# Performance work log

Measured on AMD Instinct MI355X. Metric: run time of the kernel, lower is better.

Reference implementation:

```python
import jax, jax.numpy as jnp
import numpy as np

N_NODES = 100000
N_EDGES = 1600000
DIM = 128
K_LAYERS = 3


def setup_inputs() -> dict:
    key = jax.random.key(0)
    ks = jax.random.split(key, 6)
    x = jax.random.normal(ks[0], (N_NODES, DIM), dtype=jnp.float32)
    edge_index = jax.random.randint(ks[1], (2, N_EDGES), 0, N_NODES, dtype=jnp.int64)
    scale = 1.0 / np.sqrt(DIM)
    W1 = jax.random.normal(ks[2], (K_LAYERS, DIM, DIM), dtype=jnp.float32) * scale
    b1 = jnp.zeros((K_LAYERS, DIM), dtype=jnp.float32)
    W2 = jax.random.normal(ks[3], (K_LAYERS, DIM, DIM), dtype=jnp.float32) * scale
    b2 = jnp.zeros((K_LAYERS, DIM), dtype=jnp.float32)
    return {"x": x, "edge_index": edge_index, "W1": W1, "b1": b1, "W2": W2, "b2": b2}


def reference(x, edge_index, W1, b1, W2, b2):
    # GINConv (PyG, eps=0): out = MLP(x + sum_{j -> i} x_j)
    src = edge_index[0]  # message source nodes (x_j)
    dst = edge_index[1]  # aggregation targets
    n = x.shape[0]
    for i in range(K_LAYERS):
        agg = jax.ops.segment_sum(x[src], dst, num_segments=n)  # [N, D]
        h = x + agg                                             # (1+eps)*x + agg, eps=0
        h = jax.nn.relu(h @ W1[i] + b1[i])
        x = h @ W2[i] + b2[i]
    return x
```

## Files before the change

kernel.cpp:

```cpp
#include <hip/hip_runtime.h>
#include <hip/hip_bf16.h>
#include <cstddef>

#define DIM_C 128
typedef unsigned short ushort_t;
typedef unsigned int uint_t;

constexpr int TILE_N = 64;
constexpr int BLOCK  = 256;
constexpr int HP2    = DIM_C + 8;
constexpr int CAP    = 64;

typedef __attribute__((ext_vector_type(8))) short bf16x8;
typedef __attribute__((ext_vector_type(4))) float f32x4;
typedef int intx4 __attribute__((ext_vector_type(4)));

__device__ inline ushort_t f2bf(float x) {
    __hip_bfloat16 h = __float2bfloat16(x);
    return *reinterpret_cast<ushort_t*>(&h);
}

constexpr int NGRP   = 8;
constexpr int NCHUNK = 256;
constexpr int NB_BKT = NGRP * NCHUNK;

__global__ __launch_bounds__(256)
void prep_all(const int* __restrict__ srcv, const int* __restrict__ dstv,
              int E, int N, int* __restrict__ cnt, int* __restrict__ col,
              const float* __restrict__ x, ushort_t* __restrict__ xb,
              const float* __restrict__ W1, const float* __restrict__ W2,
              ushort_t* __restrict__ Wt1, ushort_t* __restrict__ Wt2,
              int n8, int per)
{
    if (blockIdx.x < NB_BKT) {
        const int grp   = blockIdx.x & (NGRP - 1);
        const int chunk = blockIdx.x >> 3;
        const int RW = (N + NGRP - 1) / NGRP;
        const int lo = grp * RW;
        const int Q  = E >> 2;
        const int QP = (Q + NCHUNK - 1) / NCHUNK;
        const int q0 = chunk * QP;
        const int q1 = min(Q, q0 + QP);
        const intx4* d4p = (const intx4*)dstv;
        const intx4* s4p = (const intx4*)srcv;

        for (int q = q0 + threadIdx.x; q < q1; q += 256) {
            intx4 d = __builtin_nontemporal_load(&d4p[q]);
            const bool a0 = (unsigned)(d.x - lo) < (unsigned)RW;
            const bool a1 = (unsigned)(d.y - lo) < (unsigned)RW;
            const bool a2 = (unsigned)(d.z - lo) < (unsigned)RW;
            const bool a3 = (unsigned)(d.w - lo) < (unsigned)RW;
            if (a0 | a1 | a2 | a3) {
                intx4 s = __builtin_nontemporal_load(&s4p[q]);
                int p;
                if (a0) { p = atomicAdd(&cnt[d.x], 1); if (p < CAP) col[(size_t)d.x * CAP + p] = s.x; }
                if (a1) { p = atomicAdd(&cnt[d.y], 1); if (p < CAP) col[(size_t)d.y * CAP + p] = s.y; }
                if (a2) { p = atomicAdd(&cnt[d.z], 1); if (p < CAP) col[(size_t)d.z * CAP + p] = s.z; }
                if (a3) { p = atomicAdd(&cnt[d.w], 1); if (p < CAP) col[(size_t)d.w * CAP + p] = s.w; }
            }
        }
        if (chunk == 0) {
            for (int e = (Q << 2) + threadIdx.x; e < E; e += 256) {
                int dd = dstv[e];
                if ((unsigned)(dd - lo) < (unsigned)RW) {
                    int p = atomicAdd(&cnt[dd], 1);
                    if (p < CAP) col[(size_t)dd * CAP + p] = srcv[e];
                }
            }
        }
    } else {
        int i = (blockIdx.x - NB_BKT) * 256 + threadIdx.x;
        if (i < n8) {
            float4 a = ((const float4*)x)[2 * i];
            float4 b = ((const float4*)x)[2 * i + 1];
            union { ushort_t us[8]; uint4 u; } pk;
            pk.us[0] = f2bf(a.x); pk.us[1] = f2bf(a.y); pk.us[2] = f2bf(a.z); pk.us[3] = f2bf(a.w);
            pk.us[4] = f2bf(b.x); pk.us[5] = f2bf(b.y); pk.us[6] = f2bf(b.z); pk.us[7] = f2bf(b.w);
            ((uint4*)xb)[i] = pk.u;
        } else {
            int idx = i - n8;
            if (idx < 2 * per) {
                const float* src = (idx < per) ? W1 : W2;
                ushort_t* dst    = (idx < per) ? Wt1 : Wt2;
                int r = (idx < per) ? idx : idx - per;
                int l = r >> 14, rr = r & 16383, n = rr >> 7, k = rr & 127;
                dst[r] = f2bf(src[(l << 14) + (k << 7) + n]);
            }
        }
    }
}

__device__ inline void acc_bf8(float* acc, uint4 v) {
    uint_t w[4] = {v.x, v.y, v.z, v.w};
    #pragma unroll
    for (int k = 0; k < 4; ++k) {
        acc[2 * k]     += __uint_as_float(w[k] << 16);
        acc[2 * k + 1] += __uint_as_float(w[k] & 0xffff0000u);
    }
}

template <int U>
__device__ inline void gq(float* acc, const ushort_t* __restrict__ xb,
                          int cc, int qb, int j, int lq) {
    int cs[U];
    #pragma unroll
    for (int u = 0; u < U; ++u) cs[u] = __shfl(cc, qb + j + u);
    uint4 v[U];
    #pragma unroll
    for (int u = 0; u < U; ++u)
        v[u] = ((const uint4*)(xb + (size_t)cs[u] * DIM_C))[lq];
    #pragma unroll
    for (int u = 0; u < U; ++u) acc_bf8(acc, v[u]);
}

__device__ inline void ld4(uint4* v, const ushort_t* __restrict__ xb,
                           int cc, int qb, int j, int lq) {
    #pragma unroll
    for (int u = 0; u < 4; ++u) {
        int cs = __shfl(cc, qb + j + u);
        v[u] = ((const uint4*)(xb + (size_t)cs * DIM_C))[lq];
    }
}
__device__ inline void ac4(float* acc, const uint4* v) {
    #pragma unroll
    for (int u = 0; u < 4; ++u) acc_bf8(acc, v[u]);
}

__global__ __launch_bounds__(BLOCK, 4)
void gin_layer(const ushort_t* __restrict__ xb,
               const int* __restrict__ cnt,
               const int* __restrict__ col,
               const ushort_t* __restrict__ Wt1, const float* __restrict__ b1,
               const ushort_t* __restrict__ Wt2, const float* __restrict__ b2,
               float* __restrict__ xout_f, ushort_t* __restrict__ xout_b,
               int n_nodes)
{
    __shared__ __align__(16) ushort_t hb16[TILE_N * HP2];

    const int tid  = threadIdx.x;
    const int wave = tid >> 6;
    const int lane = tid & 63;
    const int q    = lane >> 4;
    const int lq   = lane & 15;
    const int qb   = 16 * q;
    const int node0 = blockIdx.x * TILE_N;
    const int w16   = wave * 16;

    {
        int cl = 0;
        if (lane < 16) {
            int nd = node0 + w16 + lane;
            cl = (nd < n_nodes) ? cnt[nd] : 0;
        }
        int n0s = min(node0 + w16 + q, n_nodes - 1);
        int c0 = col[(size_t)n0s * CAP + lq];
        int c1 = col[(size_t)n0s * CAP + 16 + lq];

        for (int i = 0; i < 4; ++i) {
            const int ln = w16 + i * 4 + q;
            const int n  = node0 + ln;
            const int nsafe = min(n, n_nodes - 1);
            const int cq = min(__shfl(cl, i * 4 + q), CAP);

            int cn0 = 0, cn1 = 0;
            if (i < 3) {
                int n1s = min(node0 + w16 + (i + 1) * 4 + q, n_nodes - 1);
                cn0 = col[(size_t)n1s * CAP + lq];
                cn1 = col[(size_t)n1s * CAP + 16 + lq];
            }

            float acc[8] = {0.f, 0.f, 0.f, 0.f, 0.f, 0.f, 0.f, 0.f};
            if (n < n_nodes) {
                uint4 sv = ((const uint4*)(xb + (size_t)n * DIM_C))[lq];
                acc_bf8(acc, sv);
            }

            for (int blk = 0; blk < 4; ++blk) {
                int mq = cq - blk * 16;
                mq = max(0, min(mq, 16));
                if (!__any(mq > 0)) break;
                int cc = (blk == 0) ? c0 : (blk == 1) ? c1
                         : col[(size_t)nsafe * CAP + blk * 16 + lq];
                if (mq == 16) {
                    uint4 va[4], vb[4];
                    ld4(va, xb, cc, qb, 0,  lq);
                    ld4(vb, xb, cc, qb, 4,  lq);
                    ac4(acc, va);
                    ld4(va, xb, cc, qb, 8,  lq);
                    ac4(acc, vb);
                    ld4(vb, xb, cc, qb, 12, lq);
                    ac4(acc, va);
                    ac4(acc, vb);
                } else {
                    int j = 0;
                    if (mq >= 8) {
                        uint4 va[4], vb[4];
                        ld4(va, xb, cc, qb, 0, lq);
                        ld4(vb, xb, cc, qb, 4, lq);
                        ac4(acc, va);
                        ac4(acc, vb);
                        j = 8;
                    }
                    if (j + 4 <= mq) { gq<4>(acc, xb, cc, qb, j, lq); j += 4; }
                    if (j + 2 <= mq) { gq<2>(acc, xb, cc, qb, j, lq); j += 2; }
                    if (j < mq)      { gq<1>(acc, xb, cc, qb, j, lq); }
                }
            }

            union { ushort_t us[8]; uint4 u; } pk;
            #pragma unroll
            for (int k = 0; k < 8; ++k) pk.us[k] = f2bf(acc[k]);
            *(uint4*)&hb16[ln * HP2 + 8 * lq] = pk.u;

            c0 = cn0; c1 = cn1;
        }
    }

    const int ml   = lane & 15;
    const int quad = lane >> 4;

    f32x4 acc1[8];
    #pragma unroll
    for (int nn = 0; nn < 8; ++nn) {
        float bv = b1[nn * 16 + ml];
        f32x4 a; a[0] = bv; a[1] = bv; a[2] = bv; a[3] = bv;
        acc1[nn] = a;
    }
    #pragma unroll
    for (int kk = 0; kk < 4; ++kk) {
        bf16x8 af = *(const bf16x8*)&hb16[(w16 + ml) * HP2 + kk * 32 + quad * 8];
        #pragma unroll
        for (int nn = 0; nn < 8; ++nn) {
            bf16x8 bf = *(const bf16x8*)&Wt1[(size_t)(nn * 16 + ml) * DIM_C + kk * 32 + quad * 8];
            acc1[nn] = __builtin_amdgcn_mfma_f32_16x16x32_bf16(af, bf, acc1[nn], 0, 0, 0);
        }
    }
    #pragma unroll
    for (int nn = 0; nn < 8; ++nn) {
        #pragma unroll
        for (int r = 0; r < 4; ++r) {
            hb16[(w16 + quad * 4 + r) * HP2 + nn * 16 + ml] = f2bf(fmaxf(acc1[nn][r], 0.f));
        }
    }

    f32x4 acc2[8];
    #pragma unroll
    for (int nn = 0; nn < 8; ++nn) {
        float bv = b2[nn * 16 + ml];
        f32x4 a; a[0] = bv; a[1] = bv; a[2] = bv; a[3] = bv;
        acc2[nn] = a;
    }
    #pragma unroll
    for (int kk = 0; kk < 4; ++kk) {
        bf16x8 af = *(const bf16x8*)&hb16[(w16 + ml) * HP2 + kk * 32 + quad * 8];
        #pragma unroll
        for (int nn = 0; nn < 8; ++nn) {
            bf16x8 bf = *(const bf16x8*)&Wt2[(size_t)(nn * 16 + ml) * DIM_C + kk * 32 + quad * 8];
            acc2[nn] = __builtin_amdgcn_mfma_f32_16x16x32_bf16(af, bf, acc2[nn], 0, 0, 0);
        }
    }

    #pragma unroll
    for (int nn = 0; nn < 8; ++nn) {
        #pragma unroll
        for (int r = 0; r < 4; ++r) {
            const int node = node0 + w16 + quad * 4 + r;
            if (node < n_nodes) {
                if (xout_f) xout_f[(size_t)node * DIM_C + nn * 16 + ml] = acc2[nn][r];
                else        xout_b[(size_t)node * DIM_C + nn * 16 + ml] = f2bf(acc2[nn][r]);
            }
        }
    }
}

extern "C" void kernel_launch(void* const* d_in, const int* in_sizes, int n_in,
                              void* d_out, int out_size, void* d_ws, size_t ws_size,
                              hipStream_t stream) {
    const float* x  = (const float*)d_in[0];
    const int* eidx = (const int*)d_in[1];
    const float* W1 = (const float*)d_in[2];
    const float* b1 = (const float*)d_in[3];
    const float* W2 = (const float*)d_in[4];
    const float* b2 = (const float*)d_in[5];
    float* out = (float*)d_out;

    const int N = in_sizes[0] / DIM_C;
    const int E = in_sizes[1] / 2;

    ushort_t* xb0 = (ushort_t*)d_ws;
    int* cnt      = (int*)(xb0 + (size_t)N * DIM_C);
    int* col      = cnt + N;
    ushort_t* Wt1 = (ushort_t*)(col + (size_t)N * CAP);
    ushort_t* Wt2 = Wt1 + 3 * DIM_C * DIM_C;
    ushort_t* xb1 = (ushort_t*)d_out;

    const int* srcv = eidx;
    const int* dstv = eidx + E;

    const int n8  = N * DIM_C / 8;
    const int per = 3 * DIM_C * DIM_C;
    const int nCvt = (n8 + 2 * per + 255) / 256;

    hipMemsetAsync(cnt, 0, (size_t)N * sizeof(int), stream);
    prep_all<<<NB_BKT + nCvt, 256, 0, stream>>>(srcv, dstv, E, N, cnt, col,
                                                x, xb0, W1, W2, Wt1, Wt2, n8, per);

    const int nblk = (N + TILE_N - 1) / TILE_N;
    const int WS = DIM_C * DIM_C;
    gin_layer<<<nblk, BLOCK, 0, stream>>>(xb0, cnt, col, Wt1,          b1,       Wt2,          b2,       nullptr, xb1, N);
    gin_layer<<<nblk, BLOCK, 0, stream>>>(xb1, cnt, col, Wt1 + WS,     b1 + 128, Wt2 + WS,     b2 + 128, nullptr, xb0, N);
    gin_layer<<<nblk, BLOCK, 0, stream>>>(xb0, cnt, col, Wt1 + 2 * WS, b1 + 256, Wt2 + 2 * WS, b2 + 256, out, nullptr, N);
}
```

Baseline: 522.3 us.

## Transpose MLP MFMA operands, shrink tile to 32 nodes, vectorize stores

Measured after the change: 815.9 us. 56.2% more time.

```diff
diff --git a/kernel.cpp b/kernel.cpp
--- a/kernel.cpp
+++ b/kernel.cpp
@@ -6,8 +6,8 @@
 typedef unsigned short ushort_t;
 typedef unsigned int uint_t;
 
-constexpr int TILE_N = 64;
-constexpr int BLOCK  = 256;
+constexpr int TILE_N = 32;
+constexpr int BLOCK  = 128;
 constexpr int HP2    = DIM_C + 8;
 constexpr int CAP    = 64;
 
@@ -126,7 +126,7 @@
     for (int u = 0; u < 4; ++u) acc_bf8(acc, v[u]);
 }
 
-__global__ __launch_bounds__(BLOCK, 4)
+__global__ __launch_bounds__(BLOCK, 6)
 void gin_layer(const ushort_t* __restrict__ xb,
                const int* __restrict__ cnt,
                const int* __restrict__ col,
@@ -218,56 +218,53 @@
 
     const int ml   = lane & 15;
     const int quad = lane >> 4;
-
-    f32x4 acc1[8];
-    #pragma unroll
-    for (int nn = 0; nn < 8; ++nn) {
-        float bv = b1[nn * 16 + ml];
-        f32x4 a; a[0] = bv; a[1] = bv; a[2] = bv; a[3] = bv;
-        acc1[nn] = a;
-    }
-    #pragma unroll
-    for (int kk = 0; kk < 4; ++kk) {
-        bf16x8 af = *(const bf16x8*)&hb16[(w16 + ml) * HP2 + kk * 32 + quad * 8];
+    const int rowo = (w16 + ml) * HP2;
+
+    bf16x8 af0 = *(const bf16x8*)&hb16[rowo +  0 + quad * 8];
+    bf16x8 af1 = *(const bf16x8*)&hb16[rowo + 32 + quad * 8];
+    bf16x8 af2 = *(const bf16x8*)&hb16[rowo + 64 + quad * 8];
+    bf16x8 af3 = *(const bf16x8*)&hb16[rowo + 96 + quad * 8];
+
+    {
+        const ushort_t* w1p = Wt1 + (size_t)ml * DIM_C + quad * 8;
         #pragma unroll
         for (int nn = 0; nn < 8; ++nn) {
-            bf16x8 bf = *(const bf16x8*)&Wt1[(size_t)(nn * 16 + ml) * DIM_C + kk * 32 + quad * 8];
-            acc1[nn] = __builtin_amdgcn_mfma_f32_16x16x32_bf16(af, bf, acc1[nn], 0, 0, 0);
-        }
-    }
-    #pragma unroll
-    for (int nn = 0; nn < 8; ++nn) {
-        #pragma unroll
-        for (int r = 0; r < 4; ++r) {
-            hb16[(w16 + quad * 4 + r) * HP2 + nn * 16 + ml] = f2bf(fmaxf(acc1[nn][r], 0.f));
-        }
-    }
-
-    f32x4 acc2[8];
-    #pragma unroll
-    for (int nn = 0; nn < 8; ++nn) {
-        float bv = b2[nn * 16 + ml];
-        f32x4 a; a[0] = bv; a[1] = bv; a[2] = bv; a[3] = bv;
-        acc2[nn] = a;
-    }
-    #pragma unroll
-    for (int kk = 0; kk < 4; ++kk) {
-        bf16x8 af = *(const bf16x8*)&hb16[(w16 + ml) * HP2 + kk * 32 + quad * 8];
+            f32x4 acc = *(const f32x4*)&b1[nn * 16 + quad * 4];
+            const ushort_t* wp = w1p + (size_t)(nn * 16) * DIM_C;
+            acc = __builtin_amdgcn_mfma_f32_16x16x32_bf16(*(const bf16x8*)&wp[0],  af0, acc, 0, 0, 0);
+            acc = __builtin_amdgcn_mfma_f32_16x16x32_bf16(*(const bf16x8*)&wp[32], af1, acc, 0, 0, 0);
+            acc = __builtin_amdgcn_mfma_f32_16x16x32_bf16(*(const bf16x8*)&wp[64], af2, acc, 0, 0, 0);
+            acc = __builtin_amdgcn_mfma_f32_16x16x32_bf16(*(const bf16x8*)&wp[96], af3, acc, 0, 0, 0);
+            uint_t lo = (uint_t)f2bf(fmaxf(acc[0], 0.f)) | ((uint_t)f2bf(fmaxf(acc[1], 0.f)) << 16);
+            uint_t hi = (uint_t)f2bf(fmaxf(acc[2], 0.f)) | ((uint_t)f2bf(fmaxf(acc[3], 0.f)) << 16);
+            *(uint2*)&hb16[rowo + nn * 16 + quad * 4] = make_uint2(lo, hi);
+        }
+    }
+
+    {
+        bf16x8 ag0 = *(const bf16x8*)&hb16[rowo +  0 + quad * 8];
+        bf16x8 ag1 = *(const bf16x8*)&hb16[rowo + 32 + quad * 8];
+        bf16x8 ag2 = *(const bf16x8*)&hb16[rowo + 64 + quad * 8];
+        bf16x8 ag3 = *(const bf16x8*)&hb16[rowo + 96 + quad * 8];
+
+        const ushort_t* w2p = Wt2 + (size_t)ml * DIM_C + quad * 8;
+        const int node = node0 + w16 + ml;
         #pragma unroll
         for (int nn = 0; nn < 8; ++nn) {
-            bf16x8 bf = *(const bf16x8*)&Wt2[(size_t)(nn * 16 + ml) * DIM_C + kk * 32 + quad * 8];
-            acc2[nn] = __builtin_amdgcn_mfma_f32_16x16x32_bf16(af, bf, acc2[nn], 0, 0, 0);
-        }
-    }
-
-    #pragma unroll
-    for (int nn = 0; nn < 8; ++nn) {
-        #pragma unroll
-        for (int r = 0; r < 4; ++r) {
-            const int node = node0 + w16 + quad * 4 + r;
+            f32x4 acc = *(const f32x4*)&b2[nn * 16 + quad * 4];
+            const ushort_t* wp = w2p + (size_t)(nn * 16) * DIM_C;
+            acc = __builtin_amdgcn_mfma_f32_16x16x32_bf16(*(const bf16x8*)&wp[0],  ag0, acc, 0, 0, 0);
+            acc = __builtin_amdgcn_mfma_f32_16x16x32_bf16(*(const bf16x8*)&wp[32], ag1, acc, 0, 0, 0);
+            acc = __builtin_amdgcn_mfma_f32_16x16x32_bf16(*(const bf16x8*)&wp[64], ag2, acc, 0, 0, 0);
+            acc = __builtin_amdgcn_mfma_f32_16x16x32_bf16(*(const bf16x8*)&wp[96], ag3, acc, 0, 0, 0);
             if (node < n_nodes) {
-                if (xout_f) xout_f[(size_t)node * DIM_C + nn * 16 + ml] = acc2[nn][r];
-                else        xout_b[(size_t)node * DIM_C + nn * 16 + ml] = f2bf(acc2[nn][r]);
+                if (xout_f) {
+                    *(f32x4*)&xout_f[(size_t)node * DIM_C + nn * 16 + quad * 4] = acc;
+                } else {
+                    uint_t lo = (uint_t)f2bf(acc[0]) | ((uint_t)f2bf(acc[1]) << 16);
+                    uint_t hi = (uint_t)f2bf(acc[2]) | ((uint_t)f2bf(acc[3]) << 16);
+                    *(uint2*)&xout_b[(size_t)node * DIM_C + nn * 16 + quad * 4] = make_uint2(lo, hi);
+                }
             }
         }
     }
```
